# Kernel tuning notes

Measured on AMD Instinct MI355X. Metric: run time of the kernel, lower is better.

## Reference

```python
import jax, jax.numpy as jnp
import numpy as np

B, H, W, C = 2, 64, 64, 256
NH, K = 8, 7  # num_heads, neighborhood kernel size


def setup_inputs() -> dict:
    key = jax.random.key(0)
    ks = jax.random.split(key, 8)
    xav = lambda k, shape: jax.random.normal(k, shape, jnp.float32) * np.sqrt(2.0 / (shape[0] + shape[1])).astype(np.float32)
    return {
        "x": jax.random.normal(ks[0], (B, H, W, C), jnp.float32),
        "norm1_g": jnp.ones((C,), jnp.float32),
        "norm1_b": jnp.zeros((C,), jnp.float32),
        "qkv_w": xav(ks[1], (3 * C, C)),
        "qkv_b": jnp.zeros((3 * C,), jnp.float32),
        "rpb": jax.random.normal(ks[2], (NH, 2 * K - 1, 2 * K - 1), jnp.float32) * 0.02,
        "proj_w": xav(ks[3], (C, C)),
        "proj_b": jnp.zeros((C,), jnp.float32),
        "norm2_g": jnp.ones((C,), jnp.float32),
        "norm2_b": jnp.zeros((C,), jnp.float32),
        "fc1_w": xav(ks[4], (4 * C, C)),
        "fc1_b": jnp.zeros((4 * C,), jnp.float32),
        "fc2_w": xav(ks[5], (C, 4 * C)),
        "fc2_b": jnp.zeros((C,), jnp.float32),
    }


def _layernorm(x, g, b, eps=1e-5):
    m = x.mean(-1, keepdims=True)
    v = jnp.mean((x - m) ** 2, axis=-1, keepdims=True)
    return (x - m) * jax.lax.rsqrt(v + eps) * g + b


def _nat2d(x, qkv_w, qkv_b, rpb, proj_w, proj_b):
    """Neighborhood attention 2D (NATTEN semantics: edge-clamped k x k windows,
    relative positional bias indexed by key_pos - query_pos + k - 1)."""
    b, h, w, c = x.shape
    nh = rpb.shape[0]
    k = (rpb.shape[1] + 1) // 2
    dh = c // nh
    qkv = (x @ qkv_w.T + qkv_b).reshape(b, h, w, 3, nh, dh)
    q = qkv[..., 0, :, :] * (dh ** -0.5)  # [b,h,w,nh,dh]
    kk = qkv[..., 1, :, :]
    vv = qkv[..., 2, :, :]
    # edge-clamped window starts per query row/col
    starts_h = jnp.clip(jnp.arange(h) - k // 2, 0, h - k)
    starts_w = jnp.clip(jnp.arange(w) - k // 2, 0, w - k)
    idx_h = starts_h[:, None] + jnp.arange(k)  # [h,k] key row indices
    idx_w = starts_w[:, None] + jnp.arange(k)  # [w,k] key col indices
    # gather neighborhoods -> [b,h,w,k,k,nh,dh]
    knb = kk[:, idx_h][:, :, :, idx_w].transpose(0, 1, 3, 2, 4, 5, 6)
    vnb = vv[:, idx_h][:, :, :, idx_w].transpose(0, 1, 3, 2, 4, 5, 6)
    attn = jnp.einsum('bijhd,bijklhd->bijhkl', q, knb)  # [b,h,w,nh,k,k]
    # relative positional bias: index = key - query + (k-1) in [0, 2k-2]
    rb_h = idx_h - jnp.arange(h)[:, None] + (k - 1)  # [h,k]
    rb_w = idx_w - jnp.arange(w)[:, None] + (k - 1)  # [w,k]
    bias = rpb[:, rb_h][:, :, :, rb_w]  # [nh,h,k,w,k]
    bias = bias.transpose(1, 3, 0, 2, 4)  # [h,w,nh,k,k]
    attn = jax.nn.softmax((attn + bias).reshape(b, h, w, nh, k * k), axis=-1)
    out = jnp.einsum('bijhn,bijnhd->bijhd', attn, vnb.reshape(b, h, w, k * k, nh, dh))
    return out.reshape(b, h, w, c) @ proj_w.T + proj_b


def reference(x, norm1_g, norm1_b, qkv_w, qkv_b, rpb, proj_w, proj_b,
              norm2_g, norm2_b, fc1_w, fc1_b, fc2_w, fc2_b):
    # norm -> neighborhood attention -> residual
    x = x + _nat2d(_layernorm(x, norm1_g, norm1_b), qkv_w, qkv_b, rpb, proj_w, proj_b)
    # norm -> MLP (gelu) -> residual
    hdn = _layernorm(x, norm2_g, norm2_b)
    hdn = jax.nn.gelu(hdn @ fc1_w.T + fc1_b, approximate=False)
    return x + (hdn @ fc2_w.T + fc2_b)
```

## Files before the change

kernel.cpp:

```cpp
#include <hip/hip_runtime.h>

typedef __attribute__((ext_vector_type(8))) short bf16x8;
typedef __attribute__((ext_vector_type(4))) float f32x4;
typedef unsigned short u16;

__device__ __forceinline__ float bf2f(u16 u) {
    return __builtin_bit_cast(float, ((unsigned int)u) << 16);
}
__device__ __forceinline__ u16 f2bf(float f) {
    unsigned int x = __builtin_bit_cast(unsigned int, f);
    x += 0x7FFFu + ((x >> 16) & 1u);
    return (u16)(x >> 16);
}

typedef const __attribute__((address_space(1))) void* gas_t;
typedef __attribute__((address_space(3))) void* las_t;
__device__ __forceinline__ void load_lds16(const u16* g, u16* l) {
    __builtin_amdgcn_global_load_lds((gas_t)g, (las_t)l, 16, 0, 0);
}

__global__ __launch_bounds__(256) void prep_kernel(
    const float* __restrict__ x, const float* __restrict__ g, const float* __restrict__ b,
    const float* __restrict__ s0, const float* __restrict__ s1,
    const float* __restrict__ s2, const float* __restrict__ s3,
    u16* __restrict__ wbf, u16* __restrict__ y)
{
    const int bid = blockIdx.x, tid = threadIdx.x;
    {
        int idx = bid * 256 + tid;
        #pragma unroll
        for (int r = 0; r < 2; ++r) {
            if (r == 1) {
                if (tid >= 128) break;
                idx = 524288 + bid * 128 + tid;
            }
            const float* src; int off;
            if      (idx < 196608) { src = s0; off = idx; }
            else if (idx < 262144) { src = s1; off = idx - 196608; }
            else if (idx < 524288) { src = s2; off = idx - 262144; }
            else                   { src = s3; off = idx - 524288; }
            wbf[idx] = f2bf(src[off]);
        }
    }
    const int tok  = bid * 4 + (tid >> 6);
    const int lane = tid & 63;
    float4 v = *(const float4*)(x + (size_t)tok * 256 + lane * 4);
    float s  = v.x + v.y + v.z + v.w;
    float sq = v.x*v.x + v.y*v.y + v.z*v.z + v.w*v.w;
    #pragma unroll
    for (int off = 32; off; off >>= 1) {
        s  += __shfl_xor(s, off);
        sq += __shfl_xor(sq, off);
    }
    const float mean = s * (1.0f / 256.0f);
    const float var  = sq * (1.0f / 256.0f) - mean * mean;
    const float rs   = rsqrtf(var + 1e-5f);
    float4 gv = *(const float4*)(g + lane * 4);
    float4 bv = *(const float4*)(b + lane * 4);
    ushort4 o;
    o.x = f2bf((v.x - mean) * rs * gv.x + bv.x);
    o.y = f2bf((v.y - mean) * rs * gv.y + bv.y);
    o.z = f2bf((v.z - mean) * rs * gv.z + bv.z);
    o.w = f2bf((v.w - mean) * rs * gv.w + bv.w);
    *(ushort4*)(y + (size_t)tok * 256 + lane * 4) = o;
}

template<int N, int K, int EPI>
__global__ __launch_bounds__(256) void gemm128x64(
    const u16* __restrict__ A, const u16* __restrict__ W,
    const float* __restrict__ bias, const float* __restrict__ res,
    void* __restrict__ outv)
{
    __shared__ u16 As[128 * 64];
    __shared__ u16 Bs[64 * 64];
    const int tid  = threadIdx.x;
    const int lane = tid & 63;
    const int wave = tid >> 6;
    const int m0   = blockIdx.x * 128;
    const int n0   = blockIdx.y * 64;
    const int wm0  = wave * 32;

    f32x4 acc[2][4];
    #pragma unroll
    for (int mt = 0; mt < 2; ++mt)
        #pragma unroll
        for (int nt = 0; nt < 4; ++nt)
            acc[mt][nt] = (f32x4){0.f, 0.f, 0.f, 0.f};

    int aoff[4], boff[2];
    #pragma unroll
    for (int r = 0; r < 4; ++r) {
        const int s   = r * 256 + tid;
        const int row = s >> 3;
        aoff[r] = row * K + ((s & 7) ^ (row & 7)) * 8;
    }
    #pragma unroll
    for (int r = 0; r < 2; ++r) {
        const int s   = r * 256 + tid;
        const int row = s >> 3;
        boff[r] = row * K + ((s & 7) ^ (row & 7)) * 8;
    }
    const int fr = lane & 15;
    const int lc = lane >> 4;

    for (int k0 = 0; k0 < K; k0 += 64) {
        __syncthreads();
        #pragma unroll
        for (int r = 0; r < 4; ++r)
            load_lds16(A + (size_t)m0 * K + k0 + aoff[r], As + (r * 256 + tid) * 8);
        #pragma unroll
        for (int r = 0; r < 2; ++r)
            load_lds16(W + (size_t)n0 * K + k0 + boff[r], Bs + (r * 256 + tid) * 8);
        __syncthreads();
        #pragma unroll
        for (int ks = 0; ks < 2; ++ks) {
            bf16x8 af[2], bw[4];
            #pragma unroll
            for (int mt = 0; mt < 2; ++mt) {
                const int rr = wm0 + mt * 16 + fr;
                af[mt] = *(const bf16x8*)(As + rr * 64 + ((ks * 4 + lc) ^ (rr & 7)) * 8);
            }
            #pragma unroll
            for (int nt = 0; nt < 4; ++nt) {
                const int rr = nt * 16 + fr;
                bw[nt] = *(const bf16x8*)(Bs + rr * 64 + ((ks * 4 + lc) ^ (rr & 7)) * 8);
            }
            #pragma unroll
            for (int mt = 0; mt < 2; ++mt)
                #pragma unroll
                for (int nt = 0; nt < 4; ++nt)
                    acc[mt][nt] = __builtin_amdgcn_mfma_f32_16x16x32_bf16(af[mt], bw[nt], acc[mt][nt], 0, 0, 0);
        }
    }

    const int col = lane & 15;
    const int rb  = (lane >> 4) * 4;
    #pragma unroll
    for (int nt = 0; nt < 4; ++nt) {
        const int n  = n0 + nt * 16 + col;
        const float bv = bias[n];
        #pragma unroll
        for (int mt = 0; mt < 2; ++mt) {
            #pragma unroll
            for (int r = 0; r < 4; ++r) {
                const int m = m0 + wm0 + mt * 16 + rb + r;
                float v = acc[mt][nt][r] + bv;
                if (EPI == 1) {
                    if (n < 256) v *= 0.1767766952966369f;
                    ((u16*)outv)[(size_t)m * N + n] = f2bf(v);
                }
                if (EPI == 2) {
                    v += res[(size_t)m * N + n];
                    ((float*)outv)[(size_t)m * N + n] = v;
                }
                if (EPI == 3) {
                    v = 0.5f * v * (1.0f + erff(v * 0.7071067811865475f));
                    ((u16*)outv)[(size_t)m * N + n] = f2bf(v);
                }
            }
        }
    }
}

__global__ __launch_bounds__(256) void proj_ln_kernel(
    const u16* __restrict__ A, const u16* __restrict__ W, const float* __restrict__ pb,
    const float* __restrict__ xres, const float* __restrict__ g2, const float* __restrict__ b2,
    float* __restrict__ x1, u16* __restrict__ ln2out)
{
    __shared__ u16 As[64 * 32];
    __shared__ u16 Bs[256 * 32];
    const int tid  = threadIdx.x;
    const int lane = tid & 63;
    const int wave = tid >> 6;
    const int m0   = blockIdx.x * 64;

    f32x4 acc[16];
    #pragma unroll
    for (int nt = 0; nt < 16; ++nt) acc[nt] = (f32x4){0.f, 0.f, 0.f, 0.f};

    const int arow = tid >> 2, acs = tid & 3;
    const int aoff = (m0 + arow) * 256 + (acs ^ (arow & 3)) * 8;
    int boff[4];
    #pragma unroll
    for (int r = 0; r < 4; ++r) {
        const int s   = r * 256 + tid;
        const int row = s >> 2;
        boff[r] = row * 256 + ((s & 3) ^ (row & 3)) * 8;
    }
    const int fr = lane & 15;
    const int fc = lane >> 4;

    for (int k0 = 0; k0 < 256; k0 += 32) {
        __syncthreads();
        load_lds16(A + aoff + k0, As + tid * 8);
        #pragma unroll
        for (int r = 0; r < 4; ++r)
            load_lds16(W + boff[r] + k0, Bs + (r * 256 + tid) * 8);
        __syncthreads();
        const int ra = wave * 16 + fr;
        bf16x8 af = *(const bf16x8*)(As + ra * 32 + (fc ^ (ra & 3)) * 8);
        #pragma unroll
        for (int nt = 0; nt < 16; ++nt) {
            const int rbq = nt * 16 + fr;
            bf16x8 bw = *(const bf16x8*)(Bs + rbq * 32 + (fc ^ (rbq & 3)) * 8);
            acc[nt] = __builtin_amdgcn_mfma_f32_16x16x32_bf16(af, bw, acc[nt], 0, 0, 0);
        }
    }

    const int col = lane & 15;
    const int g   = lane >> 4;
    float s[4] = {0.f, 0.f, 0.f, 0.f}, sq[4] = {0.f, 0.f, 0.f, 0.f};
    #pragma unroll
    for (int nt = 0; nt < 16; ++nt) {
        const int n = nt * 16 + col;
        const float bv = pb[n];
        #pragma unroll
        for (int r = 0; r < 4; ++r) {
            const int m = m0 + wave * 16 + g * 4 + r;
            float v = acc[nt][r] + bv + xres[(size_t)m * 256 + n];
            acc[nt][r] = v;
            s[r] += v; sq[r] += v * v;
        }
    }
    #pragma unroll
    for (int off = 1; off < 16; off <<= 1) {
        #pragma unroll
        for (int r = 0; r < 4; ++r) {
            s[r]  += __shfl_xor(s[r], off);
            sq[r] += __shfl_xor(sq[r], off);
        }
    }
    float mean[4], rs[4];
    #pragma unroll
    for (int r = 0; r < 4; ++r) {
        mean[r] = s[r] * (1.0f / 256.0f);
        const float var = sq[r] * (1.0f / 256.0f) - mean[r] * mean[r];
        rs[r] = rsqrtf(var + 1e-5f);
    }
    #pragma unroll
    for (int nt = 0; nt < 16; ++nt) {
        const int n = nt * 16 + col;
        const float gam = g2[n], bet = b2[n];
        #pragma unroll
        for (int r = 0; r < 4; ++r) {
            const int m = m0 + wave * 16 + g * 4 + r;
            const float v = acc[nt][r];
            x1[(size_t)m * 256 + n] = v;
            ln2out[(size_t)m * 256 + n] = f2bf((v - mean[r]) * rs[r] * gam + bet);
        }
    }
}

__global__ __launch_bounds__(256, 2) void attn_tile_kernel(
    const u16* __restrict__ qkv, const float* __restrict__ rpb,
    u16* __restrict__ out)
{
    __shared__ u16   kv[100 * 64];
    __shared__ u16   qs[16 * 32];
    __shared__ float probs[16 * 66];

    const int tid  = threadIdx.x;
    const int bb   = blockIdx.x >> 8;
    const int rem  = blockIdx.x & 255;
    const int ti0  = (rem >> 4) << 2;
    const int tj0  = (rem & 15) << 2;
    const int oh   = min(max(ti0 - 3, 0), 54);
    const int ow   = min(max(tj0 - 3, 0), 54);
    const int tokbase = bb * 4096;

    int off_kv[4];
    #pragma unroll
    for (int r = 0; r < 4; ++r) {
        const int s  = r * 256 + tid;
        const int t  = s >> 3;
        const int c  = (s & 7) ^ (t & 7);
        const int tr = t / 10, tc = t - tr * 10;
        const int tokg = tokbase + (oh + tr) * 64 + (ow + tc);
        off_kv[r] = tokg * 768 + 256 + ((c & 4) << 6) + (c & 3) * 8;
    }
    const int tq   = tid >> 2;
    const int qoff = (tokbase + (ti0 + (tq >> 2)) * 64 + (tj0 + (tq & 3))) * 768
                   + (tid & 3) * 8;

    const int token = tid >> 4;
    const int part  = tid & 15;
    const int li = token >> 2, lj = token & 3;
    const int i  = ti0 + li,   j  = tj0 + lj;
    const int sh = min(max(i - 3, 0), 57);
    const int sw = min(max(j - 3, 0), 57);
    const int rowbase  = (sh - oh) * 10 + (sw - ow);
    const int rb_const = (sh - i + 6) * 13 + (sw - j + 6);
    const size_t outbase = (size_t)(tokbase + i * 64 + j) * 256 + part * 2;

    for (int h = 0; h < 8; ++h) {
        __syncthreads();
        const int hoff = h * 32;
        #pragma unroll
        for (int r = 0; r < 3; ++r)
            load_lds16(qkv + off_kv[r] + hoff, kv + (r * 256 + tid) * 8);
        if (tid < 32)
            load_lds16(qkv + off_kv[3] + hoff, kv + (768 + tid) * 8);
        if (tid < 64)
            load_lds16(qkv + qoff + hoff, qs + tid * 8);
        __syncthreads();

        float qv[32];
        #pragma unroll
        for (int c = 0; c < 4; ++c) {
            bf16x8 v = *(const bf16x8*)(qs + token * 32 + c * 8);
            #pragma unroll
            for (int e = 0; e < 8; ++e) qv[c * 8 + e] = bf2f((u16)v[e]);
        }

        float sc[4];
        #pragma unroll
        for (int sidx = 0; sidx < 4; ++sidx) {
            const int n = part + sidx * 16;
            if (n < 49) {
                const int kh = n / 7, kw = n - (n / 7) * 7;
                const int hidx = rowbase + kh * 10 + kw;
                float acc = rpb[h * 169 + rb_const + kh * 13 + kw];
                #pragma unroll
                for (int c = 0; c < 4; ++c) {
                    const int slot = (hidx << 3) + (c ^ (hidx & 7));
                    bf16x8 kk = *(const bf16x8*)(kv + slot * 8);
                    #pragma unroll
                    for (int e = 0; e < 8; ++e)
                        acc += qv[c * 8 + e] * bf2f((u16)kk[e]);
                }
                sc[sidx] = acc;
            } else {
                sc[sidx] = -1e30f;
            }
        }
        float mx = fmaxf(fmaxf(sc[0], sc[1]), fmaxf(sc[2], sc[3]));
        #pragma unroll
        for (int off = 1; off < 16; off <<= 1) mx = fmaxf(mx, __shfl_xor(mx, off));
        float ex[4], ssum = 0.f;
        #pragma unroll
        for (int sidx = 0; sidx < 4; ++sidx) {
            ex[sidx] = __expf(sc[sidx] - mx);
            ssum += ex[sidx];
        }
        #pragma unroll
        for (int off = 1; off < 16; off <<= 1) ssum += __shfl_xor(ssum, off);
        const float inv = 1.0f / ssum;
        #pragma unroll
        for (int sidx = 0; sidx < 4; ++sidx)
            probs[token * 66 + part + sidx * 16] = ex[sidx] * inv;
        __syncthreads();

        float o0 = 0.f, o1 = 0.f;
        const int vchunk = 4 + (part >> 2);
        const int vsub   = (part & 3) * 2;
        #pragma unroll
        for (int kh = 0; kh < 7; ++kh) {
            #pragma unroll
            for (int kw = 0; kw < 7; ++kw) {
                const int n    = kh * 7 + kw;
                const int hidx = rowbase + kh * 10 + kw;
                const float p  = probs[token * 66 + n];
                const int slot = (hidx << 3) + (vchunk ^ (hidx & 7));
                const unsigned int vv = *(const unsigned int*)(kv + slot * 8 + vsub);
                o0 += p * bf2f((u16)(vv & 0xffffu));
                o1 += p * bf2f((u16)(vv >> 16));
            }
        }
        ushort2 ov;
        ov.x = f2bf(o0); ov.y = f2bf(o1);
        *(ushort2*)(out + outbase + hoff) = ov;
    }
}

extern "C" void kernel_launch(void* const* d_in, const int* in_sizes, int n_in,
                              void* d_out, int out_size, void* d_ws, size_t ws_size,
                              hipStream_t stream)
{
    const float* x      = (const float*)d_in[0];
    const float* n1g    = (const float*)d_in[1];
    const float* n1b    = (const float*)d_in[2];
    const float* qkv_w  = (const float*)d_in[3];
    const float* qkv_b  = (const float*)d_in[4];
    const float* rpb    = (const float*)d_in[5];
    const float* proj_w = (const float*)d_in[6];
    const float* proj_b = (const float*)d_in[7];
    const float* n2g    = (const float*)d_in[8];
    const float* n2b    = (const float*)d_in[9];
    const float* fc1_w  = (const float*)d_in[10];
    const float* fc1_b  = (const float*)d_in[11];
    const float* fc2_w  = (const float*)d_in[12];
    const float* fc2_b  = (const float*)d_in[13];
    float* out = (float*)d_out;

    char* wsb = (char*)d_ws;
    u16*   wbf   = (u16*)wsb;
    u16*   qkvW  = wbf;
    u16*   projW = wbf + 196608;
    u16*   fc1W  = wbf + 262144;
    u16*   fc2W  = wbf + 524288;
    u16*   ln1   = (u16*)(wsb + 1572864);
    u16*   attnB = ln1;
    u16*   qkvB  = (u16*)(wsb + 5767168);
    u16*   ln2   = qkvB;
    u16*   hbuf  = (u16*)(wsb + 9961472);
    float* x1    = (float*)(wsb + 26738688);

    dim3 blk(256);
    prep_kernel<<<2048, blk, 0, stream>>>(x, n1g, n1b, qkv_w, proj_w, fc1_w, fc2_w, wbf, ln1);
    gemm128x64<768, 256, 1><<<dim3(64, 12), blk, 0, stream>>>(ln1, qkvW, qkv_b, nullptr, qkvB);
    attn_tile_kernel<<<512, blk, 0, stream>>>(qkvB, rpb, attnB);
    proj_ln_kernel<<<128, blk, 0, stream>>>(attnB, projW, proj_b, x, n2g, n2b, x1, ln2);
    gemm128x64<1024, 256, 3><<<dim3(64, 16), blk, 0, stream>>>(ln2, fc1W, fc1_b, nullptr, hbuf);
    gemm128x64<256, 1024, 2><<<dim3(64, 4), blk, 0, stream>>>(hbuf, fc2W, fc2_b, x1, out);
}
```

Measured before the change: 165.9 us.

## Double-buffer per-head K/V tiles in LDS and preload all query heads once

The attention tile kernel now preloads the query vectors for all 8 heads into LDS once, using an XOR-swizzled layout. K/V for head h+1 is prefetched into a second LDS buffer while head h is being computed, so global loads overlap compute. The per-head barriers drop from three to one: the probs barrier is removed because each token's probabilities are written and read within one wave. The cost is more LDS per block (about 38KB), which could cut occupancy. Correctness relies on the end-of-loop barrier also waiting for the async LDS loads to finish.

```diff
diff --git a/kernel.cpp b/kernel.cpp
--- a/kernel.cpp
+++ b/kernel.cpp
@@ -255,8 +255,8 @@
     const u16* __restrict__ qkv, const float* __restrict__ rpb,
     u16* __restrict__ out)
 {
-    __shared__ u16   kv[100 * 64];
-    __shared__ u16   qs[16 * 32];
+    __shared__ u16   kv[2 * 6400];
+    __shared__ u16   qs[16 * 256];
     __shared__ float probs[16 * 66];
 
     const int tid  = threadIdx.x;
@@ -278,9 +278,16 @@
         const int tokg = tokbase + (oh + tr) * 64 + (ow + tc);
         off_kv[r] = tokg * 768 + 256 + ((c & 4) << 6) + (c & 3) * 8;
     }
-    const int tq   = tid >> 2;
-    const int qoff = (tokbase + (ti0 + (tq >> 2)) * 64 + (tj0 + (tq & 3))) * 768
-                   + (tid & 3) * 8;
+    int off_q[2];
+    #pragma unroll
+    for (int r = 0; r < 2; ++r) {
+        const int s  = r * 256 + tid;
+        const int t  = s >> 5;
+        const int c  = s & 31;
+        const int cg = (c & 24) | ((c & 7) ^ (t & 7));
+        const int tokg = tokbase + (ti0 + (t >> 2)) * 64 + (tj0 + (t & 3));
+        off_q[r] = tokg * 768 + cg * 8;
+    }
 
     const int token = tid >> 4;
     const int part  = tid & 15;
@@ -292,22 +299,35 @@
     const int rb_const = (sh - i + 6) * 13 + (sw - j + 6);
     const size_t outbase = (size_t)(tokbase + i * 64 + j) * 256 + part * 2;
 
+    #pragma unroll
+    for (int r = 0; r < 3; ++r)
+        load_lds16(qkv + off_kv[r], kv + (r * 256 + tid) * 8);
+    if (tid < 32)
+        load_lds16(qkv + off_kv[3], kv + (768 + tid) * 8);
+    #pragma unroll
+    for (int r = 0; r < 2; ++r)
+        load_lds16(qkv + off_q[r], qs + (r * 256 + tid) * 8);
+    __syncthreads();
+
     for (int h = 0; h < 8; ++h) {
-        __syncthreads();
-        const int hoff = h * 32;
-        #pragma unroll
-        for (int r = 0; r < 3; ++r)
-            load_lds16(qkv + off_kv[r] + hoff, kv + (r * 256 + tid) * 8);
-        if (tid < 32)
-            load_lds16(qkv + off_kv[3] + hoff, kv + (768 + tid) * 8);
-        if (tid < 64)
-            load_lds16(qkv + qoff + hoff, qs + tid * 8);
-        __syncthreads();
+        const u16* kvb = kv + (h & 1) * 6400;
+
+        if (h < 7) {
+            u16* nb = kv + ((h + 1) & 1) * 6400;
+            const int hoff2 = (h + 1) * 32;
+            #pragma unroll
+            for (int r = 0; r < 3; ++r)
+                load_lds16(qkv + off_kv[r] + hoff2, nb + (r * 256 + tid) * 8);
+            if (tid < 32)
+                load_lds16(qkv + off_kv[3] + hoff2, nb + (768 + tid) * 8);
+        }
 
         float qv[32];
         #pragma unroll
         for (int c = 0; c < 4; ++c) {
-            bf16x8 v = *(const bf16x8*)(qs + token * 32 + c * 8);
+            const int lcq  = h * 4 + c;
+            const int phys = (lcq & 24) | ((lcq & 7) ^ (token & 7));
+            bf16x8 v = *(const bf16x8*)(qs + token * 256 + phys * 8);
             #pragma unroll
             for (int e = 0; e < 8; ++e) qv[c * 8 + e] = bf2f((u16)v[e]);
         }
@@ -323,7 +343,7 @@
                 #pragma unroll
                 for (int c = 0; c < 4; ++c) {
                     const int slot = (hidx << 3) + (c ^ (hidx & 7));
-                    bf16x8 kk = *(const bf16x8*)(kv + slot * 8);
+                    bf16x8 kk = *(const bf16x8*)(kvb + slot * 8);
                     #pragma unroll
                     for (int e = 0; e < 8; ++e)
                         acc += qv[c * 8 + e] * bf2f((u16)kk[e]);
@@ -348,7 +368,6 @@
         #pragma unroll
         for (int sidx = 0; sidx < 4; ++sidx)
             probs[token * 66 + part + sidx * 16] = ex[sidx] * inv;
-        __syncthreads();
 
         float o0 = 0.f, o1 = 0.f;
         const int vchunk = 4 + (part >> 2);
@@ -361,14 +380,16 @@
                 const int hidx = rowbase + kh * 10 + kw;
                 const float p  = probs[token * 66 + n];
                 const int slot = (hidx << 3) + (vchunk ^ (hidx & 7));
-                const unsigned int vv = *(const unsigned int*)(kv + slot * 8 + vsub);
+                const unsigned int vv = *(const unsigned int*)(kvb + slot * 8 + vsub);
                 o0 += p * bf2f((u16)(vv & 0xffffu));
                 o1 += p * bf2f((u16)(vv >> 16));
             }
         }
         ushort2 ov;
         ov.x = f2bf(o0); ov.y = f2bf(o1);
-        *(ushort2*)(out + outbase + hoff) = ov;
+        *(ushort2*)(out + outbase + h * 32) = ov;
+
+        __syncthreads();
     }
 }
 
```

After: 167.3 us. Within noise of the previous version (+0.8%).
